# Performance work log

Hardware: AMD Instinct MI355X
Metric: run time of the kernel (lower is better)

The kernel has to match this reference:

```python
import jax, jax.numpy as jnp
import numpy as np

BLOCK = 128      # ModelArgs.block_size
FP8_MAX = 448.0  # e4m3 max, used by act_quant


def setup_inputs() -> dict:
    key = jax.random.key(0)
    k1, k2, k3 = jax.random.split(key, 3)
    M, K, O = 8192, 4096, 4096
    x = jax.random.normal(k1, (M, K), dtype=jnp.float32)
    # 'fp8' weight values (simulated in fp32) and blockwise fp32 scales
    weight = jax.random.normal(k2, (O, K), dtype=jnp.float32)
    w_scale = jax.random.uniform(k3, (O // BLOCK, K // BLOCK), dtype=jnp.float32,
                                 minval=0.5, maxval=1.5)
    return {"x": x, "weight": weight, "w_scale": w_scale}


def reference(x, weight, w_scale):
    M, K = x.shape
    O = weight.shape[0]
    Kb, Ob = K // BLOCK, O // BLOCK

    # --- act_quant: per-(row, k-block) scale = amax/448, quantized vals x/scale ---
    xb = x.reshape(M, Kb, BLOCK)
    sx = jnp.max(jnp.abs(xb), axis=-1, keepdims=True) / FP8_MAX  # [M, Kb, 1]
    xq = xb / sx                                                  # simulated fp8 activations

    # --- weight_dequant: blockwise scale expansion ---
    wdq = (weight.reshape(Ob, BLOCK, Kb, BLOCK) * w_scale[:, None, :, None]).reshape(O, K)

    # --- fp8_gemm: y = (xq * sx) @ wdq^T  (activation scales folded back per block) ---
    xd = (xq * sx).reshape(M, K)
    y = jnp.einsum('mk,ok->mo', xd, wdq)  # [M, O]
    return y
```

## Files before the change

kernel.cpp:

```cpp
#include <hip/hip_runtime.h>

#define M_DIM 8192
#define K_DIM 4096
#define O_DIM 4096
#define QB    128
#define BK    64
#define BMT   256
#define BNT   256

typedef __attribute__((ext_vector_type(8))) short  short8;
typedef __attribute__((ext_vector_type(4))) float  floatx4;

#define AS1 __attribute__((address_space(1)))
#define AS3 __attribute__((address_space(3)))

__device__ __forceinline__ short f2bf(float f) {
    unsigned u = __float_as_uint(f);
    unsigned r = u + 0x7fffu + ((u >> 16) & 1u);
    return (short)(r >> 16);
}

__global__ __launch_bounds__(512) void cvt_fused(const float* __restrict__ x,
                                                 const float* __restrict__ w,
                                                 const float* __restrict__ s,
                                                 short* __restrict__ xb,
                                                 short* __restrict__ wb) {
    const size_t NX = (size_t)M_DIM * K_DIM / 8;
    size_t t = (size_t)blockIdx.x * 512 + threadIdx.x;
    if (t < NX) {
        size_t i = t * 8;
        floatx4 f0 = *(const floatx4*)(x + i);
        floatx4 f1 = *(const floatx4*)(x + i + 4);
        short8 o;
        o[0] = f2bf(f0[0]); o[1] = f2bf(f0[1]); o[2] = f2bf(f0[2]); o[3] = f2bf(f0[3]);
        o[4] = f2bf(f1[0]); o[5] = f2bf(f1[1]); o[6] = f2bf(f1[2]); o[7] = f2bf(f1[3]);
        *(short8*)(xb + i) = o;
    } else {
        size_t i = (t - NX) * 8;
        int o = (int)(i >> 12);
        int k = (int)(i & (K_DIM - 1));
        float sc = s[(o >> 7) * (K_DIM / QB) + (k >> 7)];
        floatx4 f0 = *(const floatx4*)(w + i);
        floatx4 f1 = *(const floatx4*)(w + i + 4);
        short8 v;
        v[0] = f2bf(f0[0] * sc); v[1] = f2bf(f0[1] * sc);
        v[2] = f2bf(f0[2] * sc); v[3] = f2bf(f0[3] * sc);
        v[4] = f2bf(f1[0] * sc); v[5] = f2bf(f1[1] * sc);
        v[6] = f2bf(f1[2] * sc); v[7] = f2bf(f1[3] * sc);
        *(short8*)(wb + i) = v;
    }
}

#define WAIT_LGKM asm volatile("s_waitcnt lgkmcnt(0)" ::: "memory")
#define WAIT_VM4  asm volatile("s_waitcnt vmcnt(4)" ::: "memory")
#define WAIT_VM0  asm volatile("s_waitcnt vmcnt(0)" ::: "memory")
#define BARR      __builtin_amdgcn_s_barrier()
#define SCHEDB    __builtin_amdgcn_sched_barrier(0)

#define LDA4(DST, BUF, ROFF)                                                    \
    _Pragma("unroll")                                                           \
    for (int mi = 0; mi < 4; ++mi) {                                            \
        DST[mi][0] = *(const short8*)&lsA[BUF][rA + (ROFF) + mi * 1024 + pc0];  \
        DST[mi][1] = *(const short8*)&lsA[BUF][rA + (ROFF) + mi * 1024 + pc1];  \
    }

#define LDB2(DST, BUF, ROFF)                                                    \
    _Pragma("unroll")                                                           \
    for (int ni = 0; ni < 2; ++ni) {                                            \
        DST[ni][0] = *(const short8*)&lsB[BUF][rB + (ROFF) + ni * 1024 + pc0];  \
        DST[ni][1] = *(const short8*)&lsB[BUF][rB + (ROFF) + ni * 1024 + pc1];  \
    }

#define MM16(AF, BF, MO, NO)                                                    \
    _Pragma("unroll")                                                           \
    for (int mi = 0; mi < 4; ++mi)                                              \
        _Pragma("unroll")                                                       \
        for (int ni = 0; ni < 2; ++ni)                                          \
            _Pragma("unroll")                                                   \
            for (int ks = 0; ks < 2; ++ks)                                      \
                acc[(MO) + mi][(NO) + ni] = __builtin_amdgcn_mfma_f32_16x16x32_bf16( \
                    AF[mi][ks], BF[ni][ks], acc[(MO) + mi][(NO) + ni], 0, 0, 0);

#define STAGE(LS, BUF, GP, KOFF, H)                                             \
    __builtin_amdgcn_global_load_lds(                                           \
        (const AS1 void*)((GP) + (size_t)((H) * 128) * K_DIM + (KOFF)),         \
        (AS3 void*)&LS[BUF][(H) * 128 * BK + dst], 16, 0, 0);                   \
    __builtin_amdgcn_global_load_lds(                                           \
        (const AS1 void*)((GP) + (size_t)((H) * 128 + 64) * K_DIM + (KOFF)),    \
        (AS3 void*)&LS[BUF][((H) * 128 + 64) * BK + dst], 16, 0, 0);

#define MFMA_PH(...)                                                            \
    BARR;                                                                       \
    WAIT_LGKM;                                                                  \
    SCHEDB;                                                                     \
    __builtin_amdgcn_s_setprio(1);                                              \
    __VA_ARGS__                                                                 \
    __builtin_amdgcn_s_setprio(0);                                              \
    BARR;                                                                       \
    SCHEDB;

__global__ __launch_bounds__(512, 2) void gemm_bt(const short* __restrict__ A,
                                                  const short* __restrict__ B,
                                                  float* __restrict__ C) {
    __shared__ __align__(16) short lsA[2][BMT * BK];
    __shared__ __align__(16) short lsB[2][BNT * BK];

    const int tid  = threadIdx.x;
    const int lane = tid & 63;
    const int wave = tid >> 6;
    const int wr   = wave >> 2;
    const int wc   = wave & 3;

    const int id  = blockIdx.x;
    const int xcd = id & 7;
    const int j   = id >> 3;
    const int bm  = j >> 1;
    const int bn  = (xcd << 1) | (j & 1);

    const int sr  = tid >> 3;
    const int csw = ((tid & 7) ^ (sr & 7)) << 3;
    const int dst = tid * 8;
    const short* gA = A + (size_t)(bm * BMT + sr) * K_DIM + csw;
    const short* gB = B + (size_t)(bn * BNT + sr) * K_DIM + csw;

    const int frow = lane & 15;
    const int fc   = lane >> 4;
    const int fsw  = frow & 7;
    const int pc0  = (fc ^ fsw) << 3;
    const int pc1  = ((4 + fc) ^ fsw) << 3;
    const int rA   = (wr * 128 + frow) * BK;
    const int rB   = (wc * 64 + frow) * BK;

    floatx4 acc[8][4];
#pragma unroll
    for (int mi = 0; mi < 8; ++mi)
#pragma unroll
        for (int ni = 0; ni < 4; ++ni)
            acc[mi][ni] = (floatx4){0.f, 0.f, 0.f, 0.f};

    short8 a0[4][2], a1[4][2], b0[2][2], b1[2][2];

    STAGE(lsA, 0, gA, 0, 0)
    STAGE(lsA, 0, gA, 0, 1)
    STAGE(lsB, 0, gB, 0, 0)
    STAGE(lsB, 0, gB, 0, 1)
    STAGE(lsA, 1, gA, 64, 0)
    STAGE(lsA, 1, gA, 64, 1)
    WAIT_VM4;
    BARR;
    SCHEDB;

#pragma unroll 1
    for (int it = 0; it < 31; ++it) {
        LDA4(a0, 0, 0)
        LDB2(b0, 0, 0)
        STAGE(lsB, 1, gB, 64, 0)
        MFMA_PH(MM16(a0, b0, 0, 0))

        LDA4(a1, 0, 4096)
        LDB2(b1, 0, 2048)
        STAGE(lsB, 1, gB, 64, 1)
        MFMA_PH(MM16(a0, b1, 0, 2))

        STAGE(lsA, 0, gA, 128, 0)
        MFMA_PH(MM16(a1, b0, 4, 0))

        STAGE(lsA, 0, gA, 128, 1)
        WAIT_VM4;
        MFMA_PH(MM16(a1, b1, 4, 2))

        LDA4(a0, 1, 0)
        LDB2(b0, 1, 0)
        STAGE(lsB, 0, gB, 128, 0)
        MFMA_PH(MM16(a0, b0, 0, 0))

        LDA4(a1, 1, 4096)
        LDB2(b1, 1, 2048)
        STAGE(lsB, 0, gB, 128, 1)
        MFMA_PH(MM16(a0, b1, 0, 2))

        STAGE(lsA, 1, gA, 192, 0)
        MFMA_PH(MM16(a1, b0, 4, 0))

        STAGE(lsA, 1, gA, 192, 1)
        WAIT_VM4;
        MFMA_PH(MM16(a1, b1, 4, 2))

        gA += 2 * BK;
        gB += 2 * BK;
    }

    LDA4(a0, 0, 0)
    LDB2(b0, 0, 0)
    STAGE(lsB, 1, gB, 64, 0)
    MFMA_PH(MM16(a0, b0, 0, 0))

    LDA4(a1, 0, 4096)
    LDB2(b1, 0, 2048)
    STAGE(lsB, 1, gB, 64, 1)
    MFMA_PH(MM16(a0, b1, 0, 2))

    MFMA_PH(MM16(a1, b0, 4, 0))

    WAIT_VM0;
    MFMA_PH(MM16(a1, b1, 4, 2))

    LDA4(a0, 1, 0)
    LDB2(b0, 1, 0)
    MFMA_PH(MM16(a0, b0, 0, 0))

    LDA4(a1, 1, 4096)
    LDB2(b1, 1, 2048)
    MFMA_PH(MM16(a0, b1, 0, 2))

    MFMA_PH(MM16(a1, b0, 4, 0))

    MFMA_PH(MM16(a1, b1, 4, 2))

    const int quad  = lane >> 4;
    const int crow0 = bm * BMT + wr * 128 + quad * 4;
    const int ccol0 = bn * BNT + wc * 64 + frow;
#pragma unroll
    for (int mi = 0; mi < 8; ++mi)
#pragma unroll
        for (int ni = 0; ni < 4; ++ni) {
            float* cp = C + (size_t)(crow0 + mi * 16) * O_DIM + (ccol0 + ni * 16);
#pragma unroll
            for (int r = 0; r < 4; ++r)
                cp[(size_t)r * O_DIM] = acc[mi][ni][r];
        }
}

extern "C" void kernel_launch(void* const* d_in, const int* in_sizes, int n_in,
                              void* d_out, int out_size, void* d_ws, size_t ws_size,
                              hipStream_t stream) {
    const float* x  = (const float*)d_in[0];
    const float* w  = (const float*)d_in[1];
    const float* ws = (const float*)d_in[2];
    float* out = (float*)d_out;

    short* xb = (short*)d_ws;
    short* wb = xb + (size_t)M_DIM * K_DIM;

    const size_t total_t = ((size_t)M_DIM * K_DIM + (size_t)O_DIM * K_DIM) / 8;
    cvt_fused<<<(unsigned)(total_t / 512), 512, 0, stream>>>(x, w, ws, xb, wb);

    gemm_bt<<<(M_DIM / BMT) * (O_DIM / BNT), 512, 0, stream>>>(xb, wb, out);
}
```

Before: 510.3 us.

## Re-pipeline GEMM main loop with partial lgkmcnt waits and earlier LDS reads

Restructures the double-buffered bf16 GEMM loop so that LDS fragment reads for the next sub-tile are issued before the previous MFMA phase. Each phase now waits on partial lgkmcnt counts (12/8/0) instead of a full drain, and the global-to-LDS stage schedule is reshuffled with vmcnt(2) waits. The goal is more overlap of LDS reads and global loads with MFMA work and fewer full stalls. The risk is that the hand-tuned counter values are wrong and cause races, or that the barriers and partial waits change occupancy or register pressure.

```diff
diff --git a/kernel.cpp b/kernel.cpp
--- a/kernel.cpp
+++ b/kernel.cpp
@@ -51,11 +51,13 @@
     }
 }
 
-#define WAIT_LGKM asm volatile("s_waitcnt lgkmcnt(0)" ::: "memory")
-#define WAIT_VM4  asm volatile("s_waitcnt vmcnt(4)" ::: "memory")
-#define WAIT_VM0  asm volatile("s_waitcnt vmcnt(0)" ::: "memory")
-#define BARR      __builtin_amdgcn_s_barrier()
-#define SCHEDB    __builtin_amdgcn_sched_barrier(0)
+#define WLG12 asm volatile("s_waitcnt lgkmcnt(12)" ::: "memory")
+#define WLG8  asm volatile("s_waitcnt lgkmcnt(8)" ::: "memory")
+#define WLG0  asm volatile("s_waitcnt lgkmcnt(0)" ::: "memory")
+#define WVM2  asm volatile("s_waitcnt vmcnt(2)" ::: "memory")
+#define WVM0  asm volatile("s_waitcnt vmcnt(0)" ::: "memory")
+#define BARR  __builtin_amdgcn_s_barrier()
+#define SCHEDB __builtin_amdgcn_sched_barrier(0)
 
 #define LDA4(DST, BUF, ROFF)                                                    \
     _Pragma("unroll")                                                           \
@@ -70,6 +72,11 @@
         DST[ni][0] = *(const short8*)&lsB[BUF][rB + (ROFF) + ni * 1024 + pc0];  \
         DST[ni][1] = *(const short8*)&lsB[BUF][rB + (ROFF) + ni * 1024 + pc1];  \
     }
+
+#define RDA0(B) LDA4(a0, B, 0)
+#define RDA1(B) LDA4(a1, B, 4096)
+#define RDB0(B) LDB2(b0, B, 0)
+#define RDB1(B) LDB2(b1, B, 2048)
 
 #define MM16(AF, BF, MO, NO)                                                    \
     _Pragma("unroll")                                                           \
@@ -89,15 +96,30 @@
         (const AS1 void*)((GP) + (size_t)((H) * 128 + 64) * K_DIM + (KOFF)),    \
         (AS3 void*)&LS[BUF][((H) * 128 + 64) * BK + dst], 16, 0, 0);
 
-#define MFMA_PH(...)                                                            \
-    BARR;                                                                       \
-    WAIT_LGKM;                                                                  \
-    SCHEDB;                                                                     \
+#define PH(STAGES, WAITM, MFMAS)                                                \
+    STAGES                                                                      \
+    BARR; WAITM; SCHEDB;                                                        \
     __builtin_amdgcn_s_setprio(1);                                              \
-    __VA_ARGS__                                                                 \
+    MFMAS                                                                       \
     __builtin_amdgcn_s_setprio(0);                                              \
-    BARR;                                                                       \
-    SCHEDB;
+    BARR; SCHEDB;
+
+#define PH3(STAGES, VMW, READS, MFMAS)                                          \
+    STAGES                                                                      \
+    VMW; BARR; SCHEDB;                                                          \
+    READS                                                                       \
+    WLG12; SCHEDB;                                                              \
+    __builtin_amdgcn_s_setprio(1);                                              \
+    MFMAS                                                                       \
+    __builtin_amdgcn_s_setprio(0);                                              \
+    BARR; SCHEDB;
+
+#define TILE(c, n, k1, k2)                                                      \
+    RDB1(c); RDA1(c);                                                           \
+    PH(STAGE(lsA, n, gA, k1, 1), WLG12, MM16(a0, b0, 0, 0))                     \
+    PH(STAGE(lsB, n, gB, k1, 0), WLG8,  MM16(a0, b1, 0, 2))                     \
+    PH(STAGE(lsB, n, gB, k1, 1), WLG0,  MM16(a1, b0, 4, 0))                     \
+    PH3(STAGE(lsA, c, gA, k2, 0), WVM2, RDA0(n); RDB0(n);, MM16(a1, b1, 4, 2))
 
 __global__ __launch_bounds__(512, 2) void gemm_bt(const short* __restrict__ A,
                                                   const short* __restrict__ B,
@@ -145,77 +167,31 @@
     STAGE(lsB, 0, gB, 0, 0)
     STAGE(lsB, 0, gB, 0, 1)
     STAGE(lsA, 1, gA, 64, 0)
-    STAGE(lsA, 1, gA, 64, 1)
-    WAIT_VM4;
-    BARR;
-    SCHEDB;
+    WVM2; BARR; SCHEDB;
+    RDA0(0); RDB0(0);
 
 #pragma unroll 1
     for (int it = 0; it < 31; ++it) {
-        LDA4(a0, 0, 0)
-        LDB2(b0, 0, 0)
-        STAGE(lsB, 1, gB, 64, 0)
-        MFMA_PH(MM16(a0, b0, 0, 0))
-
-        LDA4(a1, 0, 4096)
-        LDB2(b1, 0, 2048)
-        STAGE(lsB, 1, gB, 64, 1)
-        MFMA_PH(MM16(a0, b1, 0, 2))
-
-        STAGE(lsA, 0, gA, 128, 0)
-        MFMA_PH(MM16(a1, b0, 4, 0))
-
-        STAGE(lsA, 0, gA, 128, 1)
-        WAIT_VM4;
-        MFMA_PH(MM16(a1, b1, 4, 2))
-
-        LDA4(a0, 1, 0)
-        LDB2(b0, 1, 0)
-        STAGE(lsB, 0, gB, 128, 0)
-        MFMA_PH(MM16(a0, b0, 0, 0))
-
-        LDA4(a1, 1, 4096)
-        LDB2(b1, 1, 2048)
-        STAGE(lsB, 0, gB, 128, 1)
-        MFMA_PH(MM16(a0, b1, 0, 2))
-
-        STAGE(lsA, 1, gA, 192, 0)
-        MFMA_PH(MM16(a1, b0, 4, 0))
-
-        STAGE(lsA, 1, gA, 192, 1)
-        WAIT_VM4;
-        MFMA_PH(MM16(a1, b1, 4, 2))
-
-        gA += 2 * BK;
-        gB += 2 * BK;
-    }
-
-    LDA4(a0, 0, 0)
-    LDB2(b0, 0, 0)
-    STAGE(lsB, 1, gB, 64, 0)
-    MFMA_PH(MM16(a0, b0, 0, 0))
-
-    LDA4(a1, 0, 4096)
-    LDB2(b1, 0, 2048)
-    STAGE(lsB, 1, gB, 64, 1)
-    MFMA_PH(MM16(a0, b1, 0, 2))
-
-    MFMA_PH(MM16(a1, b0, 4, 0))
-
-    WAIT_VM0;
-    MFMA_PH(MM16(a1, b1, 4, 2))
-
-    LDA4(a0, 1, 0)
-    LDB2(b0, 1, 0)
-    MFMA_PH(MM16(a0, b0, 0, 0))
-
-    LDA4(a1, 1, 4096)
-    LDB2(b1, 1, 2048)
-    MFMA_PH(MM16(a0, b1, 0, 2))
-
-    MFMA_PH(MM16(a1, b0, 4, 0))
-
-    MFMA_PH(MM16(a1, b1, 4, 2))
+        TILE(0, 1, 64, 128)
+        TILE(1, 0, 128, 192)
+        gA += 128;
+        gB += 128;
+    }
+
+    RDB1(0); RDA1(0);
+    PH(STAGE(lsA, 1, gA, 64, 1), WLG12, MM16(a0, b0, 0, 0))
+    PH(STAGE(lsB, 1, gB, 64, 0), WLG8,  MM16(a0, b1, 0, 2))
+    PH(STAGE(lsB, 1, gB, 64, 1), WLG0,  MM16(a1, b0, 4, 0))
+    PH3(, WVM0, RDA0(1); RDB0(1);, MM16(a1, b1, 4, 2))
+
+    RDB1(1); RDA1(1);
+    PH(, WLG12, MM16(a0, b0, 0, 0))
+    PH(, WLG8,  MM16(a0, b1, 0, 2))
+    PH(, WLG0,  MM16(a1, b0, 4, 0))
+    SCHEDB;
+    __builtin_amdgcn_s_setprio(1);
+    MM16(a1, b1, 4, 2)
+    __builtin_amdgcn_s_setprio(0);
 
     const int quad  = lane >> 4;
     const int crow0 = bm * BMT + wr * 128 + quad * 4;
```

Result: faster. 491.7 us (-3.6%).
